# Optimization experiments

Measured on AMD Instinct MI355X. Metric: run time of the kernel, lower is better.

Reference implementation:

```python
import jax, jax.numpy as jnp
import numpy as np

RATE = 2
KSIZE = 3          # patch size for similarity
KERNEL = 2 * RATE  # patch size for alpha scatter (4)
BN_EPS = 1e-5


def _extract_patches(x, k, s):
    """Mirror of GuidedCxtAtten.extract_patches: reflect-pad then unfold.
    x: [B,C,H,W] -> [B,Ho,Wo,C,k,k] with Ho=H//s, Wo=W//s."""
    left = (k - s + 1) // 2
    right = (k - s) // 2
    xp = jnp.pad(x, ((0, 0), (0, 0), (left, right), (left, right)), mode='reflect')
    Hp, Wp = xp.shape[2], xp.shape[3]
    Ho = (Hp - k) // s + 1
    Wo = (Wp - k) // s + 1
    ii = (jnp.arange(Ho) * s)[:, None] + jnp.arange(k)[None, :]   # [Ho,k]
    jj = (jnp.arange(Wo) * s)[:, None] + jnp.arange(k)[None, :]   # [Wo,k]
    p = xp[:, :, ii[:, :, None, None], jj[None, None, :, :]]      # [B,C,Ho,k,Wo,k]
    return p.transpose(0, 2, 4, 1, 3, 5)                          # [B,Ho,Wo,C,k,k]


def setup_inputs() -> dict:
    key = jax.random.key(0)
    ks = jax.random.split(key, 5)
    B, Cg, Ca, H, W = 4, 256, 128, 128, 128
    f = jax.random.normal(ks[0], (B, Cg, H, W), dtype=jnp.float32)
    alpha = jax.random.normal(ks[1], (B, Ca, H, W), dtype=jnp.float32)
    unknown = (jax.random.uniform(ks[2], (B, 1, H, W)) > 0.5).astype(jnp.float32)
    # guidance_conv: 1x1, Cg -> Cg//2, xavier-ish
    gc_w = jax.random.normal(ks[3], (Cg // 2, Cg), dtype=jnp.float32) * np.sqrt(2.0 / (Cg + Cg // 2))
    gc_b = jnp.zeros((Cg // 2,), dtype=jnp.float32)
    # W[0]: 1x1 conv Ca->Ca no bias; W[1]: BN with gamma=0.001, beta=0 per init
    w_w = jax.random.normal(ks[4], (Ca, Ca), dtype=jnp.float32) * np.sqrt(1.0 / Ca)
    bn_gamma = jnp.full((Ca,), 0.001, dtype=jnp.float32)
    bn_beta = jnp.zeros((Ca,), dtype=jnp.float32)
    return {"f": f, "alpha": alpha, "unknown": unknown, "gc_w": gc_w, "gc_b": gc_b,
            "w_w": w_w, "bn_gamma": bn_gamma, "bn_beta": bn_beta}


def _forward(f, alpha, unknown, gc_w, gc_b, w_w, bn_gamma, bn_beta):
    # guidance 1x1 conv
    fg = jnp.einsum('oi,bihw->bohw', gc_w, f) + gc_b[None, :, None, None]
    B, _, H, W = fg.shape
    Ca = alpha.shape[1]
    Hs, Ws = H // RATE, W // RATE
    L = Hs * Ws

    # alpha patches [B,L,Ca,4,4] (kernel=2*rate, stride=rate)
    alpha_w = _extract_patches(alpha, KERNEL, RATE).reshape(B, L, Ca, KERNEL, KERNEL)

    # nearest downsample by rate (torch nearest with scale 1/2 == strided pick)
    f_ds = fg[:, :, ::RATE, ::RATE]                # [B,Cg/2,Hs,Ws]
    unk_ds = unknown[:, :, ::RATE, ::RATE]         # [B,1,Hs,Ws]

    # similarity filter patches [B,L,C,3,3]
    w = _extract_patches(f_ds, KSIZE, 1).reshape(B, L, -1, KSIZE, KSIZE)

    # known/unknown softmax scales [B,2]
    u_mean = unk_ds.mean(axis=(2, 3))              # [B,1]
    k_mean = 1.0 - u_mean
    su = jnp.clip(jnp.sqrt(u_mean / k_mean), 0.1, 10.0)
    sk = jnp.clip(jnp.sqrt(k_mean / u_mean), 0.1, 10.0)
    softmax_scale = jnp.concatenate([su, sk], axis=1)

    # patch-mean of unknown mask -> binary patch mask [B,L]
    m = _extract_patches(unk_ds, KSIZE, 1).reshape(B, L, -1).mean(axis=2)
    mm = (m > 0.0).astype(fg.dtype)

    # l2-normalize filters per patch, then correlate against all positions.
    # Conv of reflect-padded f_ds with stride-1 3x3 patch filters == inner
    # product of normalized patches with the raw patches (same extraction).
    norm = jnp.sqrt(jnp.sum(w * w, axis=(2, 3, 4), keepdims=True))
    w_normed = w / jnp.maximum(norm, 1e-4)
    scores = jnp.einsum('bqcij,bpcij->bqp', w_normed, w)   # [B,L(q=patch),L(p=pos)]

    # known/unknown scaling per source patch q
    gate = jnp.where(mm > 0.0, su, sk)                      # [B,L]
    scores = scores * gate[:, :, None]

    # self-match suppression only for unknown patches (diagonal q == p)
    diag = jnp.arange(L)
    scores = scores.at[:, diag, diag].add(-10000.0 * mm)

    attn = jax.nn.softmax(scores, axis=1)                   # softmax over patches q

    # offsets (argmax patch per position, relative to center)
    idx = jnp.argmax(attn, axis=1)                          # [B,L]
    offsets = jnp.stack([idx // Ws, idx % Ws], axis=1).reshape(B, 2, Hs, Ws)
    offsets = offsets - jnp.array([Hs // 2, Ws // 2]).reshape(1, 2, 1, 1)

    # scatter alpha patches with attention weights: per-sample conv_transpose2d
    attn_map = attn.reshape(B, L, Hs, Ws)

    def ct(yi, wc):  # yi [L,Hs,Ws], wc [L,Ca,4,4]
        rhs = jnp.flip(wc, (2, 3)).transpose(1, 0, 2, 3)    # [Ca,L,4,4]
        pad = KERNEL - 1 - 1                                # torch padding=1
        out = jax.lax.conv_general_dilated(
            yi[None], rhs, window_strides=(1, 1),
            padding=[(pad, pad), (pad, pad)], lhs_dilation=(RATE, RATE),
            dimension_numbers=('NCHW', 'OIHW', 'NCHW'))
        return out[0]

    y = jax.vmap(ct)(attn_map, alpha_w) / 4.0               # [B,Ca,H,W]

    # W: 1x1 conv (no bias) + BatchNorm2d (training-mode batch stats)
    yw = jnp.einsum('oi,bihw->bohw', w_w, y)
    mean = yw.mean(axis=(0, 2, 3))
    var = yw.var(axis=(0, 2, 3))
    yn = (yw - mean[None, :, None, None]) * jax.lax.rsqrt(var + BN_EPS)[None, :, None, None]
    yn = yn * bn_gamma[None, :, None, None] + bn_beta[None, :, None, None]

    return yn + alpha, offsets, softmax_scale


def reference(f, alpha, unknown, gc_w, gc_b, w_w, bn_gamma, bn_beta):
    return _forward(f, alpha, unknown, gc_w, gc_b, w_w, bn_gamma, bn_beta)
```

## Files before the change

kernel.cpp:

```cpp
#include <hip/hip_runtime.h>
#include <math.h>

#define B 4
#define CG 256
#define CM 128
#define CA 128
#define H 128
#define W_ 128
#define HS 64
#define WS 64
#define L 4096
#define D1 1152
#define D2 2048
#define NPIX 65536
#define NT1 36
#define NT2 128

#define STP_F 8388608UL
#define WF_F  4718592UL
#define ZB_F  4194304UL
#define SLOT_F (STP_F + WF_F + ZB_F)

typedef unsigned short u16;
typedef __attribute__((ext_vector_type(8))) short short8v;
typedef __attribute__((ext_vector_type(4))) unsigned short u16x4;
typedef __attribute__((ext_vector_type(4))) float f32x4;

__device__ __forceinline__ float bf2f(u16 x) {
    union { unsigned int u; float f; } v; v.u = ((unsigned int)x) << 16; return v.f;
}
__device__ __forceinline__ u16 f2bf(float x) {
    union { float f; unsigned int u; } v; v.f = x;
    unsigned int r = (v.u + 0x7FFFu + ((v.u >> 16) & 1u)) >> 16;
    return (u16)r;
}
__device__ __forceinline__ void gll16(const void* g, void* l) {
    __builtin_amdgcn_global_load_lds((const __attribute__((address_space(1))) void*)g,
                                     (__attribute__((address_space(3))) void*)l, 16, 0, 0);
}
__device__ __forceinline__ int refl(int i, int n) {
    return i < 0 ? -i : (i >= n ? 2 * n - 2 - i : i);
}
__device__ __forceinline__ int swz(int row, int fq) {
    return row * 32 + ((fq ^ ((row >> 1) & 3)) * 8);
}
__device__ __forceinline__ short8v rdfrag32(const char* lds, int r, int fq) {
    return *(const short8v*)(lds + r * 64 + ((fq * 16) ^ (((r >> 1) & 3) << 4)));
}

__global__ __launch_bounds__(256) void k_conv_ds(const float* __restrict__ f,
                                                 const float* __restrict__ gw,
                                                 const float* __restrict__ gb,
                                                 float* __restrict__ fds,
                                                 float* __restrict__ ssq) {
    __shared__ float sf[CG * 64];
    __shared__ float part[4][64];
    int t = threadIdx.x;
    int hs = blockIdx.x, b = blockIdx.y;
    const float* fb = f + (size_t)b * CG * H * W_ + (2 * hs) * W_;
    for (int idx = t; idx < CG * 64; idx += 256) {
        int ci = idx >> 6, ws = idx & 63;
        sf[idx] = fb[(size_t)ci * H * W_ + 2 * ws];
    }
    __syncthreads();
    int ws = t & 63;
    int wave = __builtin_amdgcn_readfirstlane(t >> 6);
    const float* gwp = gw + (size_t)(wave * 32) * CG;
    float acc[32];
#pragma unroll
    for (int r = 0; r < 32; ++r) acc[r] = gb[wave * 32 + r];
    for (int ci = 0; ci < CG; ++ci) {
        float fv = sf[ci * 64 + ws];
#pragma unroll
        for (int r = 0; r < 32; ++r) acc[r] += gwp[r * CG + ci] * fv;
    }
    float sq = 0.f;
#pragma unroll
    for (int r = 0; r < 32; ++r) {
        int co = wave * 32 + r;
        fds[(((size_t)b * CM + co) * HS + hs) * WS + ws] = acc[r];
        sq += acc[r] * acc[r];
    }
    part[wave][ws] = sq;
    __syncthreads();
    if (t < 64)
        ssq[((size_t)b * HS + hs) * WS + t] =
            part[0][t] + part[1][t] + part[2][t] + part[3][t];
}

__global__ __launch_bounds__(256) void k_scale(const float* __restrict__ unk,
                                               float* __restrict__ suk,
                                               float* __restrict__ out2) {
    int b = blockIdx.x, t = threadIdx.x;
    __shared__ float red[256];
    float s = 0.f;
    for (int i = t; i < L; i += 256) {
        int hs = i >> 6, ws = i & 63;
        s += unk[(size_t)b * H * W_ + (2 * hs) * W_ + 2 * ws];
    }
    red[t] = s;
    __syncthreads();
    for (int o = 128; o > 0; o >>= 1) {
        if (t < o) red[t] += red[t + o];
        __syncthreads();
    }
    if (t == 0) {
        float u = red[0] / (float)L;
        float k = 1.0f - u;
        float su = sqrtf(u / k); su = fminf(fmaxf(su, 0.1f), 10.0f);
        float sk = sqrtf(k / u); sk = fminf(fmaxf(sk, 0.1f), 10.0f);
        suk[b * 2] = su; suk[b * 2 + 1] = sk;
        out2[b * 2] = su; out2[b * 2 + 1] = sk;
    }
}

__global__ __launch_bounds__(64) void k_gate(const float* __restrict__ unk,
                                             const float* __restrict__ ssq,
                                             const float* __restrict__ suk,
                                             float* __restrict__ g,
                                             float* __restrict__ dg) {
    int ws = threadIdx.x, hs = blockIdx.x, b = blockIdx.y;
    float sm = 0.f, sq = 0.f;
    for (int di = -1; di <= 1; ++di) {
        int rh = refl(hs + di, HS);
        for (int dj = -1; dj <= 1; ++dj) {
            int rw = refl(ws + dj, WS);
            sm += unk[(size_t)b * H * W_ + (2 * rh) * W_ + 2 * rw];
            sq += ssq[((size_t)b * HS + rh) * WS + rw];
        }
    }
    float mm   = (sm > 0.0f) ? 1.0f : 0.0f;
    float norm = sqrtf(sq);
    float gate = (mm > 0.0f) ? suk[2 * b] : suk[2 * b + 1];
    int q = hs * WS + ws;
    g[(size_t)b * L + q]  = gate / fmaxf(norm, 1e-4f);
    dg[(size_t)b * L + q] = -10000.0f * mm;
}

__global__ __launch_bounds__(256) void k_buildW(const float* __restrict__ fds,
                                                float* __restrict__ base, int b0) {
    int bz = blockIdx.z;
    int b  = b0 + bz;
    float* S   = base + (size_t)bz * SLOT_F;
    float* Wf  = S + STP_F;
    u16*   Whi = (u16*)(S + STP_F + WF_F);
    int ws = threadIdx.x;
    int c  = blockIdx.y * 4 + threadIdx.y;
    int hs = blockIdx.x;
    int q = hs * WS + ws;
    size_t bo = (size_t)q * D1 + c * 9;
    const float* src = fds + ((size_t)b * CM + c) * HS * WS;
#pragma unroll
    for (int i = 0; i < 3; ++i) {
        int rh = refl(hs + i - 1, HS);
#pragma unroll
        for (int j = 0; j < 3; ++j) {
            int rw = refl(ws + j - 1, WS);
            float v = src[rh * WS + rw];
            Wf[bo + i * 3 + j]  = v;
            Whi[bo + i * 3 + j] = f2bf(v);
        }
    }
}

__global__ __launch_bounds__(256) void k_gemm1(float* __restrict__ base,
                                               const float* __restrict__ g0,
                                               const float* __restrict__ dg0,
                                               int b0) {
    __shared__ u16 sA[3][128 * 32], sB[3][128 * 32];
    int bz = blockIdx.z;
    float* S = base + (size_t)bz * SLOT_F;
    u16* STP = (u16*)S;
    const u16* Whi = (const u16*)(S + STP_F + WF_F);
    const float* g  = g0  + (size_t)(b0 + bz) * L;
    const float* dg = dg0 + (size_t)(b0 + bz) * L;

    int tid = threadIdx.x;
    int wv = tid >> 6, lane = tid & 63;
    int t0 = blockIdx.x, I = 0;
    while (t0 >= 32 - I) { t0 -= 32 - I; ++I; }
    int J = I + t0;
    int pTile = I * 128, qTile = J * 128;
    int wp = (wv >> 1) * 64, wq = (wv & 1) * 64;
    int r0 = wv * 32;
    int lrow = lane >> 2;
    int csw = ((lane & 3) ^ ((lrow >> 1) & 3)) * 8;
    int fr = lane & 15, fq = lane >> 4;

    const u16* gArow = Whi + (size_t)(pTile + r0 + lrow) * D1 + csw;
    const u16* gBrow = Whi + (size_t)(qTile + r0 + lrow) * D1 + csw;

#define G1STAGE(kt, bf) do { \
    gll16(gArow + (kt) * 32, &sA[bf][r0 * 32]); \
    gll16(gArow + (kt) * 32 + (size_t)16 * D1, &sA[bf][(r0 + 16) * 32]); \
    gll16(gBrow + (kt) * 32, &sB[bf][r0 * 32]); \
    gll16(gBrow + (kt) * 32 + (size_t)16 * D1, &sB[bf][(r0 + 16) * 32]); } while (0)

    f32x4 acc[4][4];
#pragma unroll
    for (int mi = 0; mi < 4; ++mi)
#pragma unroll
        for (int ni = 0; ni < 4; ++ni)
#pragma unroll
            for (int r = 0; r < 4; ++r) acc[mi][ni][r] = 0.f;

    G1STAGE(0, 0);
    G1STAGE(1, 1);
    asm volatile("s_waitcnt vmcnt(4)" ::: "memory");
    __builtin_amdgcn_s_barrier();
    __builtin_amdgcn_sched_barrier(0);

    for (int t = 0; t < NT1; ++t) {
        int cur = t % 3;
        short8v ah[4], bh[4];
#pragma unroll
        for (int i = 0; i < 4; ++i) {
            ah[i] = *(const short8v*)&sA[cur][swz(wp + i * 16 + fr, fq)];
            bh[i] = *(const short8v*)&sB[cur][swz(wq + i * 16 + fr, fq)];
        }
        __builtin_amdgcn_s_setprio(1);
#pragma unroll
        for (int mi = 0; mi < 2; ++mi)
#pragma unroll
            for (int ni = 0; ni < 4; ++ni)
                acc[mi][ni] = __builtin_amdgcn_mfma_f32_16x16x32_bf16(ah[mi], bh[ni], acc[mi][ni], 0, 0, 0);
        __builtin_amdgcn_s_setprio(0);
        int kt2 = (t + 2 < NT1) ? (t + 2) : 0;
        G1STAGE(kt2, (t + 2) % 3);
        asm volatile("s_waitcnt vmcnt(4)" ::: "memory");
        __builtin_amdgcn_sched_barrier(0);
        __builtin_amdgcn_s_setprio(1);
#pragma unroll
        for (int mi = 2; mi < 4; ++mi)
#pragma unroll
            for (int ni = 0; ni < 4; ++ni)
                acc[mi][ni] = __builtin_amdgcn_mfma_f32_16x16x32_bf16(ah[mi], bh[ni], acc[mi][ni], 0, 0, 0);
        __builtin_amdgcn_s_setprio(0);
        __builtin_amdgcn_s_barrier();
        __builtin_amdgcn_sched_barrier(0);
    }
#undef G1STAGE

#pragma unroll
    for (int ni = 0; ni < 4; ++ni) {
        int qq = qTile + wq + ni * 16 + fr;
        float gq = g[qq];
        float dq = dg[qq];
#pragma unroll
        for (int mi = 0; mi < 4; ++mi) {
            int pB = pTile + wp + mi * 16 + fq * 4;
#pragma unroll
            for (int r = 0; r < 4; ++r) {
                int p = pB + r;
                float v = acc[mi][ni][r] * gq;
                if (p == qq) v += dq;
                STP[(size_t)p * L + qq] = f2bf(v);
            }
        }
    }
    if (I != J) {
#pragma unroll
        for (int mi = 0; mi < 4; ++mi) {
            int p0 = pTile + wp + mi * 16 + fq * 4;
            float gp0 = g[p0], gp1 = g[p0 + 1], gp2 = g[p0 + 2], gp3 = g[p0 + 3];
#pragma unroll
            for (int ni = 0; ni < 4; ++ni) {
                int qq = qTile + wq + ni * 16 + fr;
                u16x4 mv;
                mv[0] = f2bf(acc[mi][ni][0] * gp0);
                mv[1] = f2bf(acc[mi][ni][1] * gp1);
                mv[2] = f2bf(acc[mi][ni][2] * gp2);
                mv[3] = f2bf(acc[mi][ni][3] * gp3);
                *(u16x4*)(STP + (size_t)qq * L + p0) = mv;
            }
        }
    }
}

__global__ __launch_bounds__(256) void k_softmax(float* __restrict__ base,
                                                 const float* __restrict__ g0,
                                                 const float* __restrict__ dg0,
                                                 float* __restrict__ out1, int b0) {
    __shared__ float buf[L];
    __shared__ float wmax[4], wsum[4], cred[4];
    __shared__ int candList[128];
    __shared__ int candCount;
    int bz = blockIdx.y;
    int b  = b0 + bz;
    float* S = base + (size_t)bz * SLOT_F;
    u16* STP = (u16*)S;
    const float* Wf = S + STP_F;
    const float* g  = g0  + (size_t)b * L;
    const float* dg = dg0 + (size_t)b * L;

    int p = blockIdx.x, t = threadIdx.x;
    int lane = t & 63, wv = t >> 6;
    u16* rowp = STP + (size_t)p * L;

    if (t == 0) candCount = 0;
    float mx = -3.4e38f;
    for (int i = t; i < L / 8; i += 256) {
        short8v v8 = ((const short8v*)rowp)[i];
#pragma unroll
        for (int j = 0; j < 8; ++j) {
            float v = bf2f((u16)v8[j]);
            buf[i * 8 + j] = v;
            mx = fmaxf(mx, v);
        }
    }
#pragma unroll
    for (int o = 32; o > 0; o >>= 1) mx = fmaxf(mx, __shfl_xor(mx, o));
    if (lane == 0) wmax[wv] = mx;
    __syncthreads();
    float M = fmaxf(fmaxf(wmax[0], wmax[1]), fmaxf(wmax[2], wmax[3]));
    float cth = M - (fabsf(M) * 0.0625f + 1e-5f);

    float s = 0.f;
    for (int i = t; i < L; i += 256) {
        float v = buf[i];
        if (v >= cth) {
            int ix = atomicAdd(&candCount, 1);
            if (ix < 128) candList[ix] = i;
        }
        float e = __expf(v - M);
        buf[i] = e;
        s += e;
    }
#pragma unroll
    for (int o = 32; o > 0; o >>= 1) s += __shfl_xor(s, o);
    if (lane == 0) wsum[wv] = s;
    __syncthreads();
    float inv = 1.0f / (wsum[0] + wsum[1] + wsum[2] + wsum[3]);

    for (int i = t; i < L / 8; i += 256) {
        short8v o8;
#pragma unroll
        for (int j = 0; j < 8; ++j) o8[j] = (short)f2bf(buf[i * 8 + j] * inv);
        ((short8v*)rowp)[i] = o8;
    }

    int nc = candCount; if (nc > 128) nc = 128;
    int bestI;
    if (nc == 1) {
        bestI = candList[0];
    } else {
        float bestE = -3.4e38f; bestI = L;
        const float* wp_ = Wf + (size_t)p * D1;
        for (int k = 0; k < nc; ++k) {
            int cand = candList[k];
            const float* wc = Wf + (size_t)cand * D1;
            float part = 0.f;
            for (int j = t; j < D1; j += 256) part += wp_[j] * wc[j];
#pragma unroll
            for (int o = 32; o > 0; o >>= 1) part += __shfl_xor(part, o);
            if (lane == 0) cred[wv] = part;
            __syncthreads();
            float e1 = (cred[0] + cred[1] + cred[2] + cred[3]) * g[cand]
                     + (p == cand ? dg[cand] : 0.f);
            if (e1 > bestE || (e1 == bestE && cand < bestI)) { bestE = e1; bestI = cand; }
            __syncthreads();
        }
    }
    if (t == 0) {
        out1[(size_t)(b * 2 + 0) * L + p] = (float)(bestI / WS - 32);
        out1[(size_t)(b * 2 + 1) * L + p] = (float)(bestI % WS - 32);
    }
}

__global__ __launch_bounds__(256) void k_buildA(const float* __restrict__ alpha,
                                                float* __restrict__ base, int b0) {
    int bz = blockIdx.z;
    int b  = b0 + bz;
    u16* At = (u16*)(base + (size_t)bz * SLOT_F + STP_F);
    int q = blockIdx.x * 256 + threadIdx.x;
    int n = blockIdx.y;
    int hs = q >> 6, ws = q & 63;
    int c = n >> 4, ki = (n >> 2) & 3, kj = n & 3;
    int rh = refl(2 * hs + ki - 1, H);
    int rw = refl(2 * ws + kj - 1, W_);
    At[(size_t)n * L + q] = f2bf(alpha[((size_t)b * CA + c) * H * W_ + rh * W_ + rw]);
}

__global__ __launch_bounds__(512, 2) void k_gemm2(float* __restrict__ base) {
    __shared__ u16 smem[65536];
    char* sm = (char*)smem;
    int bz = blockIdx.z;
    float* S = base + (size_t)bz * SLOT_F;
    const u16* P  = (const u16*)S;
    const u16* At = (const u16*)(S + STP_F);
    u16* Z        = (u16*)(S + STP_F + WF_F);

    int tid = threadIdx.x;
    int wid = tid >> 6, lane = tid & 63;
    int wm = wid >> 2, wn = wid & 3;
    int pTile = blockIdx.x * 256, nTile = blockIdx.y * 256;
    int fr = lane & 15, fq = lane >> 4;

    int off0 = wid * 1024 + lane * 16;
    int row0 = off0 >> 6, cb0 = off0 & 63;
    int off1 = off0 + 8192;
    int row1 = off1 >> 6, cb1 = off1 & 63;
    const u16* pA0 = P  + (size_t)(pTile + row0) * L + ((cb0 ^ (((row0 >> 1) & 3) << 4)) >> 1);
    const u16* pA1 = P  + (size_t)(pTile + row1) * L + ((cb1 ^ (((row1 >> 1) & 3) << 4)) >> 1);
    const u16* pB0 = At + (size_t)(nTile + row0) * L + ((cb0 ^ (((row0 >> 1) & 3) << 4)) >> 1);
    const u16* pB1 = At + (size_t)(nTile + row1) * L + ((cb1 ^ (((row1 >> 1) & 3) << 4)) >> 1);

#define STG2(kt, bi) do { \
    char* d = sm + (bi) * 32768 + wid * 1024; \
    gll16(pA0 + (size_t)(kt) * 32, d); \
    gll16(pA1 + (size_t)(kt) * 32, d + 8192); \
    gll16(pB0 + (size_t)(kt) * 32, d + 16384); \
    gll16(pB1 + (size_t)(kt) * 32, d + 24576); } while (0)

#define PRELOAD2(fa, fb, bi) do { \
    const char* Ab_ = sm + (bi) * 32768; \
    const char* Bb_ = Ab_ + 16384; \
    _Pragma("unroll") for (int n = 0; n < 4; ++n) fb[n] = rdfrag32(Bb_, wn * 64 + n * 16 + fr, fq); \
    _Pragma("unroll") for (int m = 0; m < 8; ++m) fa[m] = rdfrag32(Ab_, wm * 128 + m * 16 + fr, fq); } while (0)

#define PHASE2(t, ca, cb, na, nb_) do { \
    const char* Abn = sm + (((t) + 1) & 3) * 32768; \
    const char* Bbn = Abn + 16384; \
    _Pragma("unroll") for (int n = 0; n < 4; ++n) nb_[n] = rdfrag32(Bbn, wn * 64 + n * 16 + fr, fq); \
    __builtin_amdgcn_s_setprio(1); \
    _Pragma("unroll") for (int m = 0; m < 4; ++m) \
        _Pragma("unroll") for (int n = 0; n < 4; ++n) \
            acc[m][n] = __builtin_amdgcn_mfma_f32_16x16x32_bf16(ca[m], cb[n], acc[m][n], 0, 0, 0); \
    __builtin_amdgcn_s_setprio(0); \
    _Pragma("unroll") for (int m = 0; m < 8; ++m) na[m] = rdfrag32(Abn, wm * 128 + m * 16 + fr, fq); \
    STG2(((t) + 3 < NT2) ? (t) + 3 : 0, ((t) + 3) & 3); \
    asm volatile("s_waitcnt vmcnt(4)" ::: "memory"); \
    __builtin_amdgcn_s_setprio(1); \
    _Pragma("unroll") for (int m = 4; m < 8; ++m) \
        _Pragma("unroll") for (int n = 0; n < 4; ++n) \
            acc[m][n] = __builtin_amdgcn_mfma_f32_16x16x32_bf16(ca[m], cb[n], acc[m][n], 0, 0, 0); \
    __builtin_amdgcn_s_setprio(0); \
    asm volatile("s_waitcnt lgkmcnt(0)" ::: "memory"); \
    __builtin_amdgcn_s_barrier(); \
    __builtin_amdgcn_sched_barrier(0); } while (0)

    f32x4 acc[8][4];
#pragma unroll
    for (int m = 0; m < 8; ++m)
#pragma unroll
        for (int n = 0; n < 4; ++n)
#pragma unroll
            for (int r = 0; r < 4; ++r) acc[m][n][r] = 0.f;

    STG2(0, 0);
    STG2(1, 1);
    STG2(2, 2);
    asm volatile("s_waitcnt vmcnt(4)" ::: "memory");
    __builtin_amdgcn_s_barrier();
    __builtin_amdgcn_sched_barrier(0);

    short8v fa0[8], fb0[4], fa1[8], fb1[4];
    PRELOAD2(fa0, fb0, 0);
    asm volatile("s_waitcnt lgkmcnt(0)" ::: "memory");
    __builtin_amdgcn_sched_barrier(0);

    for (int t = 0; t < NT2; t += 2) {
        PHASE2(t,     fa0, fb0, fa1, fb1);
        PHASE2(t + 1, fa1, fb1, fa0, fb0);
    }
#undef PHASE2
#undef PRELOAD2
#undef STG2

#pragma unroll
    for (int m = 0; m < 8; ++m)
#pragma unroll
        for (int n = 0; n < 4; ++n) {
            int nn = nTile + wn * 64 + n * 16 + fr;
#pragma unroll
            for (int r = 0; r < 4; ++r) {
                int pp = pTile + wm * 128 + m * 16 + fq * 4 + r;
                Z[(size_t)pp * D2 + nn] = f2bf(acc[m][n][r]);
            }
        }
}

__global__ __launch_bounds__(256) void k_gather(float* __restrict__ base,
                                                u16* __restrict__ yt, int b0) {
    int bz = blockIdx.z;
    int b  = b0 + bz;
    const u16* Z = (const u16*)(base + (size_t)bz * SLOT_F + STP_F + WF_F);
    int c  = threadIdx.x & 127;
    int pl = threadIdx.x >> 7;
    int w  = blockIdx.x * 2 + pl;
    int h  = blockIdx.y;
    float s = 0.f;
#pragma unroll
    for (int ki = 0; ki < 4; ++ki) {
        int num = h + 1 - ki;
        if (num < 0 || (num & 1)) continue;
        int hs = num >> 1;
        if (hs >= HS) continue;
#pragma unroll
        for (int kj = 0; kj < 4; ++kj) {
            int numw = w + 1 - kj;
            if (numw < 0 || (numw & 1)) continue;
            int wsd = numw >> 1;
            if (wsd >= WS) continue;
            s += bf2f(Z[(size_t)(hs * WS + wsd) * D2 + c * 16 + ki * 4 + kj]);
        }
    }
    int pix = h * W_ + w;
    int cs = c ^ ((pix & 7) << 3);
    yt[((size_t)b * 16384 + pix) * 128 + cs] = f2bf(0.25f * s);
}

__global__ __launch_bounds__(256) void k_cvtww(const float* __restrict__ ww,
                                               u16* __restrict__ wwbf) {
    int i = blockIdx.x * 256 + threadIdx.x;
    int o = i >> 7, c = i & 127;
    wwbf[o * 128 + (c ^ ((o & 7) << 3))] = f2bf(ww[i]);
}

__global__ __launch_bounds__(256) void k_ywgemm(const u16* __restrict__ wwbf,
                                                const u16* __restrict__ yt,
                                                float* __restrict__ yw) {
    __shared__ u16 sA[128 * 128], sB[128 * 128];
    int tid = threadIdx.x;
    int wv = tid >> 6, lane = tid & 63;
    int nTile = blockIdx.x * 128;
    int wp = (wv >> 1) * 64, wn = (wv & 1) * 64;
    int fr = lane & 15, fq = lane >> 4;

    const u16* gB = yt + (size_t)nTile * 128;
#pragma unroll
    for (int i = 0; i < 8; ++i) {
        int o = (i * 4 + wv) * 512;
        gll16(wwbf + o + lane * 8, &sA[o]);
        gll16(gB + o + lane * 8, &sB[o]);
    }
    __syncthreads();

    f32x4 acc[4][4];
#pragma unroll
    for (int mi = 0; mi < 4; ++mi)
#pragma unroll
        for (int ni = 0; ni < 4; ++ni)
#pragma unroll
            for (int r = 0; r < 4; ++r) acc[mi][ni][r] = 0.f;

#pragma unroll
    for (int ks = 0; ks < 4; ++ks) {
        int k0 = ks * 32 + fq * 8;
        short8v a[4], bb[4];
#pragma unroll
        for (int i = 0; i < 4; ++i) {
            int ra = wp + i * 16 + fr;
            a[i] = *(const short8v*)&sA[ra * 128 + (k0 ^ ((ra & 7) << 3))];
            int rb = wn + i * 16 + fr;
            bb[i] = *(const short8v*)&sB[rb * 128 + (k0 ^ ((rb & 7) << 3))];
        }
#pragma unroll
        for (int mi = 0; mi < 4; ++mi)
#pragma unroll
            for (int ni = 0; ni < 4; ++ni)
                acc[mi][ni] = __builtin_amdgcn_mfma_f32_16x16x32_bf16(a[mi], bb[ni], acc[mi][ni], 0, 0, 0);
    }

#pragma unroll
    for (int mi = 0; mi < 4; ++mi)
#pragma unroll
        for (int ni = 0; ni < 4; ++ni) {
            int gp = nTile + wn + ni * 16 + fr;
#pragma unroll
            for (int r = 0; r < 4; ++r) {
                int o = wp + mi * 16 + fq * 4 + r;
                yw[(size_t)o * NPIX + gp] = acc[mi][ni][r];
            }
        }
}

__global__ __launch_bounds__(256) void k_stats(const float* __restrict__ yw,
                                               float* __restrict__ meanvar) {
    int o = blockIdx.x, t = threadIdx.x;
    __shared__ float rs[256], rq[256];
    float s = 0.f, q = 0.f;
    const float* p = yw + (size_t)o * NPIX;
    for (int i = t; i < NPIX; i += 256) {
        float v = p[i];
        s += v;
        q += v * v;
    }
    rs[t] = s; rq[t] = q;
    __syncthreads();
    for (int off = 128; off > 0; off >>= 1) {
        if (t < off) { rs[t] += rs[t + off]; rq[t] += rq[t + off]; }
        __syncthreads();
    }
    if (t == 0) {
        float n = (float)NPIX;
        float mean = rs[0] / n;
        float var  = rq[0] / n - mean * mean;
        meanvar[o] = mean;
        meanvar[CA + o] = var;
    }
}

__global__ __launch_bounds__(256) void k_final(const float* __restrict__ yw,
                                               const float* __restrict__ meanvar,
                                               const float* __restrict__ gamma,
                                               const float* __restrict__ beta,
                                               const float* __restrict__ alpha,
                                               float* __restrict__ out0) {
    size_t i = ((size_t)blockIdx.x * 256 + threadIdx.x) * 4;
    int c = (int)((i >> 14) & 127);
    int b = (int)(i >> 21);
    int pix = (int)(i & 16383);
    float4 v = *(const float4*)(yw + (size_t)c * NPIX + b * 16384 + pix);
    float4 a = *(const float4*)(alpha + i);
    float mean = meanvar[c];
    float var  = meanvar[CA + c];
    float sc   = rsqrtf(var + 1e-5f) * gamma[c];
    float bt   = beta[c];
    float4 r;
    r.x = (v.x - mean) * sc + bt + a.x;
    r.y = (v.y - mean) * sc + bt + a.y;
    r.z = (v.z - mean) * sc + bt + a.z;
    r.w = (v.w - mean) * sc + bt + a.w;
    *(float4*)(out0 + i) = r;
}

extern "C" void kernel_launch(void* const* d_in, const int* in_sizes, int n_in,
                              void* d_out, int out_size, void* d_ws, size_t ws_size,
                              hipStream_t stream) {
    (void)in_sizes; (void)n_in; (void)out_size;
    const float* f     = (const float*)d_in[0];
    const float* alpha = (const float*)d_in[1];
    const float* unk   = (const float*)d_in[2];
    const float* gw    = (const float*)d_in[3];
    const float* gb    = (const float*)d_in[4];
    const float* ww    = (const float*)d_in[5];
    const float* gamma = (const float*)d_in[6];
    const float* beta  = (const float*)d_in[7];

    float* out0 = (float*)d_out;
    float* out1 = out0 + (size_t)B * CA * H * W_;
    float* out2 = out1 + (size_t)B * 2 * HS * WS;

    float* wsf = (float*)d_ws;
    size_t off = 0;
    float* fds     = wsf + off; off += (size_t)B * CM * HS * WS;
    float* ssq     = wsf + off; off += (size_t)B * HS * WS;
    float* gbuf    = wsf + off; off += (size_t)B * L;
    float* dgbuf   = wsf + off; off += (size_t)B * L;
    float* suk     = wsf + off; off += 64;
    float* ytF     = wsf + off; off += (size_t)NPIX * 128 / 2;
    float* wwbfF   = wsf + off; off += 8192;
    float* meanvar = wsf + off; off += 256;
    float* base    = wsf + off;

    const size_t PRE_F = off;
    int nb = (ws_size >= (PRE_F + 4 * SLOT_F) * sizeof(float)) ? 4 : 2;

    float* yw   = base;
    u16*   yt   = (u16*)ytF;
    u16*   wwbf = (u16*)wwbfF;

    k_cvtww<<<64, 256, 0, stream>>>(ww, wwbf);
    k_conv_ds<<<dim3(64, 4), 256, 0, stream>>>(f, gw, gb, fds, ssq);
    k_scale<<<4, 256, 0, stream>>>(unk, suk, out2);
    k_gate<<<dim3(64, 4), 64, 0, stream>>>(unk, ssq, suk, gbuf, dgbuf);

    for (int b0 = 0; b0 < B; b0 += nb) {
        k_buildW<<<dim3(64, 32, nb), dim3(64, 4), 0, stream>>>(fds, base, b0);
        k_gemm1<<<dim3(528, 1, nb), 256, 0, stream>>>(base, gbuf, dgbuf, b0);
        k_softmax<<<dim3(4096, nb), 256, 0, stream>>>(base, gbuf, dgbuf, out1, b0);
        k_buildA<<<dim3(16, 2048, nb), 256, 0, stream>>>(alpha, base, b0);
        k_gemm2<<<dim3(16, 8, nb), 512, 0, stream>>>(base);
        k_gather<<<dim3(64, 128, nb), 256, 0, stream>>>(base, yt, b0);
    }

    k_ywgemm<<<512, 256, 0, stream>>>(wwbf, yt, yw);
    k_stats<<<128, 256, 0, stream>>>(yw, meanvar);
    k_final<<<8192, 256, 0, stream>>>(yw, meanvar, gamma, beta, alpha, out0);
}
```

Measured before the change: 843.8 us.

## Drop fp32 patch buffer, recompute from fds, and prefetch LDS fragments in gemm1

The fp32 unfolded patch matrix Wf is no longer materialised. The softmax tie-break dot products now gather directly from the downsampled feature map using reflect indexing, which shrinks the per-sample workspace slot and removes a large fp32 write in buildW. The gemm1 main loop is restructured to keep three stages in flight and double-buffer the register fragments, loading the next tile's LDS fragments while MFMAs on the current tile run. It also adds an occupancy hint of 3 blocks per SM.

New measurement: 829.9 us. About the same (-1.7%).

```diff
diff --git a/kernel.cpp b/kernel.cpp
--- a/kernel.cpp
+++ b/kernel.cpp
@@ -17,9 +17,8 @@
 #define NT2 128
 
 #define STP_F 8388608UL
-#define WF_F  4718592UL
-#define ZB_F  4194304UL
-#define SLOT_F (STP_F + WF_F + ZB_F)
+#define RA_F  4194304UL
+#define SLOT_F (STP_F + RA_F + RA_F)
 
 typedef unsigned short u16;
 typedef __attribute__((ext_vector_type(8))) short short8v;
@@ -141,9 +140,7 @@
                                                 float* __restrict__ base, int b0) {
     int bz = blockIdx.z;
     int b  = b0 + bz;
-    float* S   = base + (size_t)bz * SLOT_F;
-    float* Wf  = S + STP_F;
-    u16*   Whi = (u16*)(S + STP_F + WF_F);
+    u16* Whi = (u16*)(base + (size_t)bz * SLOT_F + STP_F);
     int ws = threadIdx.x;
     int c  = blockIdx.y * 4 + threadIdx.y;
     int hs = blockIdx.x;
@@ -156,22 +153,20 @@
 #pragma unroll
         for (int j = 0; j < 3; ++j) {
             int rw = refl(ws + j - 1, WS);
-            float v = src[rh * WS + rw];
-            Wf[bo + i * 3 + j]  = v;
-            Whi[bo + i * 3 + j] = f2bf(v);
-        }
-    }
-}
-
-__global__ __launch_bounds__(256) void k_gemm1(float* __restrict__ base,
-                                               const float* __restrict__ g0,
-                                               const float* __restrict__ dg0,
-                                               int b0) {
+            Whi[bo + i * 3 + j] = f2bf(src[rh * WS + rw]);
+        }
+    }
+}
+
+__global__ __launch_bounds__(256, 3) void k_gemm1(float* __restrict__ base,
+                                                  const float* __restrict__ g0,
+                                                  const float* __restrict__ dg0,
+                                                  int b0) {
     __shared__ u16 sA[3][128 * 32], sB[3][128 * 32];
     int bz = blockIdx.z;
     float* S = base + (size_t)bz * SLOT_F;
     u16* STP = (u16*)S;
-    const u16* Whi = (const u16*)(S + STP_F + WF_F);
+    const u16* Whi = (const u16*)(S + STP_F);
     const float* g  = g0  + (size_t)(b0 + bz) * L;
     const float* dg = dg0 + (size_t)(b0 + bz) * L;
 
@@ -190,12 +185,34 @@
     const u16* gArow = Whi + (size_t)(pTile + r0 + lrow) * D1 + csw;
     const u16* gBrow = Whi + (size_t)(qTile + r0 + lrow) * D1 + csw;
 
-#define G1STAGE(kt, bf) do { \
+#define G1STG(kt, bf) do { \
     gll16(gArow + (kt) * 32, &sA[bf][r0 * 32]); \
     gll16(gArow + (kt) * 32 + (size_t)16 * D1, &sA[bf][(r0 + 16) * 32]); \
     gll16(gBrow + (kt) * 32, &sB[bf][r0 * 32]); \
     gll16(gBrow + (kt) * 32 + (size_t)16 * D1, &sB[bf][(r0 + 16) * 32]); } while (0)
 
+#define G1PHASE(t, ca, cb, na, nb_) do { \
+    int nxb = ((t) + 1) % 3; \
+    _Pragma("unroll") for (int i = 0; i < 4; ++i) \
+        nb_[i] = *(const short8v*)&sB[nxb][swz(wq + i * 16 + fr, fq)]; \
+    __builtin_amdgcn_s_setprio(1); \
+    _Pragma("unroll") for (int mi = 0; mi < 2; ++mi) \
+        _Pragma("unroll") for (int ni = 0; ni < 4; ++ni) \
+            acc[mi][ni] = __builtin_amdgcn_mfma_f32_16x16x32_bf16(ca[mi], cb[ni], acc[mi][ni], 0, 0, 0); \
+    __builtin_amdgcn_s_setprio(0); \
+    _Pragma("unroll") for (int i = 0; i < 4; ++i) \
+        na[i] = *(const short8v*)&sA[nxb][swz(wp + i * 16 + fr, fq)]; \
+    G1STG(((t) + 3 < NT1) ? (t) + 3 : 0, (t) % 3); \
+    asm volatile("s_waitcnt vmcnt(4)" ::: "memory"); \
+    __builtin_amdgcn_s_setprio(1); \
+    _Pragma("unroll") for (int mi = 2; mi < 4; ++mi) \
+        _Pragma("unroll") for (int ni = 0; ni < 4; ++ni) \
+            acc[mi][ni] = __builtin_amdgcn_mfma_f32_16x16x32_bf16(ca[mi], cb[ni], acc[mi][ni], 0, 0, 0); \
+    __builtin_amdgcn_s_setprio(0); \
+    asm volatile("s_waitcnt lgkmcnt(0)" ::: "memory"); \
+    __builtin_amdgcn_s_barrier(); \
+    __builtin_amdgcn_sched_barrier(0); } while (0)
+
     f32x4 acc[4][4];
 #pragma unroll
     for (int mi = 0; mi < 4; ++mi)
@@ -204,42 +221,29 @@
 #pragma unroll
             for (int r = 0; r < 4; ++r) acc[mi][ni][r] = 0.f;
 
-    G1STAGE(0, 0);
-    G1STAGE(1, 1);
+    G1STG(0, 0);
+    G1STG(1, 1);
+    G1STG(2, 2);
     asm volatile("s_waitcnt vmcnt(4)" ::: "memory");
     __builtin_amdgcn_s_barrier();
     __builtin_amdgcn_sched_barrier(0);
 
-    for (int t = 0; t < NT1; ++t) {
-        int cur = t % 3;
-        short8v ah[4], bh[4];
-#pragma unroll
-        for (int i = 0; i < 4; ++i) {
-            ah[i] = *(const short8v*)&sA[cur][swz(wp + i * 16 + fr, fq)];
-            bh[i] = *(const short8v*)&sB[cur][swz(wq + i * 16 + fr, fq)];
-        }
-        __builtin_amdgcn_s_setprio(1);
-#pragma unroll
-        for (int mi = 0; mi < 2; ++mi)
-#pragma unroll
-            for (int ni = 0; ni < 4; ++ni)
-                acc[mi][ni] = __builtin_amdgcn_mfma_f32_16x16x32_bf16(ah[mi], bh[ni], acc[mi][ni], 0, 0, 0);
-        __builtin_amdgcn_s_setprio(0);
-        int kt2 = (t + 2 < NT1) ? (t + 2) : 0;
-        G1STAGE(kt2, (t + 2) % 3);
-        asm volatile("s_waitcnt vmcnt(4)" ::: "memory");
-        __builtin_amdgcn_sched_barrier(0);
-        __builtin_amdgcn_s_setprio(1);
-#pragma unroll
-        for (int mi = 2; mi < 4; ++mi)
-#pragma unroll
-            for (int ni = 0; ni < 4; ++ni)
-                acc[mi][ni] = __builtin_amdgcn_mfma_f32_16x16x32_bf16(ah[mi], bh[ni], acc[mi][ni], 0, 0, 0);
-        __builtin_amdgcn_s_setprio(0);
-        __builtin_amdgcn_s_barrier();
-        __builtin_amdgcn_sched_barrier(0);
-    }
-#undef G1STAGE
+    short8v fa0[4], fb0[4], fa1[4], fb1[4];
+#pragma unroll
+    for (int i = 0; i < 4; ++i) {
+        fa0[i] = *(const short8v*)&sA[0][swz(wp + i * 16 + fr, fq)];
+        fb0[i] = *(const short8v*)&sB[0][swz(wq + i * 16 + fr, fq)];
+    }
+    asm volatile("s_waitcnt lgkmcnt(0)" ::: "memory");
+    __builtin_amdgcn_s_barrier();
+    __builtin_amdgcn_sched_barrier(0);
+
+    for (int t = 0; t < NT1; t += 2) {
+        G1PHASE(t,     fa0, fb0, fa1, fb1);
+        G1PHASE(t + 1, fa1, fb1, fa0, fb0);
+    }
+#undef G1PHASE
+#undef G1STG
 
 #pragma unroll
     for (int ni = 0; ni < 4; ++ni) {
@@ -278,6 +282,7 @@
 }
 
 __global__ __launch_bounds__(256) void k_softmax(float* __restrict__ base,
+                                                 const float* __restrict__ fds,
                                                  const float* __restrict__ g0,
                                                  const float* __restrict__ dg0,
                                                  float* __restrict__ out1, int b0) {
@@ -289,7 +294,7 @@
     int b  = b0 + bz;
     float* S = base + (size_t)bz * SLOT_F;
     u16* STP = (u16*)S;
-    const float* Wf = S + STP_F;
+    const float* fdsb = fds + (size_t)b * CM * HS * WS;
     const float* g  = g0  + (size_t)b * L;
     const float* dg = dg0 + (size_t)b * L;
 
@@ -345,12 +350,24 @@
         bestI = candList[0];
     } else {
         float bestE = -3.4e38f; bestI = L;
-        const float* wp_ = Wf + (size_t)p * D1;
+        int hp = p >> 6, wpp = p & 63;
         for (int k = 0; k < nc; ++k) {
             int cand = candList[k];
-            const float* wc = Wf + (size_t)cand * D1;
+            int hc = cand >> 6, wcc = cand & 63;
             float part = 0.f;
-            for (int j = t; j < D1; j += 256) part += wp_[j] * wc[j];
+#pragma unroll
+            for (int e = 0; e < 5; ++e) {
+                int kk = t + e * 256;
+                if (kk < D1) {
+                    int c  = kk / 9, ij = kk - c * 9;
+                    int di = ij / 3, dj = ij - di * 3;
+                    float pv = fdsb[(size_t)c * (HS * WS)
+                                    + refl(hp + di - 1, HS) * WS + refl(wpp + dj - 1, WS)];
+                    float cv = fdsb[(size_t)c * (HS * WS)
+                                    + refl(hc + di - 1, HS) * WS + refl(wcc + dj - 1, WS)];
+                    part += pv * cv;
+                }
+            }
 #pragma unroll
             for (int o = 32; o > 0; o >>= 1) part += __shfl_xor(part, o);
             if (lane == 0) cred[wv] = part;
@@ -388,7 +405,7 @@
     float* S = base + (size_t)bz * SLOT_F;
     const u16* P  = (const u16*)S;
     const u16* At = (const u16*)(S + STP_F);
-    u16* Z        = (u16*)(S + STP_F + WF_F);
+    u16* Z        = (u16*)(S + STP_F + RA_F);
 
     int tid = threadIdx.x;
     int wid = tid >> 6, lane = tid & 63;
@@ -484,7 +501,7 @@
                                                 u16* __restrict__ yt, int b0) {
     int bz = blockIdx.z;
     int b  = b0 + bz;
-    const u16* Z = (const u16*)(base + (size_t)bz * SLOT_F + STP_F + WF_F);
+    const u16* Z = (const u16*)(base + (size_t)bz * SLOT_F + STP_F + RA_F);
     int c  = threadIdx.x & 127;
     int pl = threadIdx.x >> 7;
     int w  = blockIdx.x * 2 + pl;
@@ -669,7 +686,7 @@
     for (int b0 = 0; b0 < B; b0 += nb) {
         k_buildW<<<dim3(64, 32, nb), dim3(64, 4), 0, stream>>>(fds, base, b0);
         k_gemm1<<<dim3(528, 1, nb), 256, 0, stream>>>(base, gbuf, dgbuf, b0);
-        k_softmax<<<dim3(4096, nb), 256, 0, stream>>>(base, gbuf, dgbuf, out1, b0);
+        k_softmax<<<dim3(4096, nb), 256, 0, stream>>>(base, fds, gbuf, dgbuf, out1, b0);
         k_buildA<<<dim3(16, 2048, nb), 256, 0, stream>>>(alpha, base, b0);
         k_gemm2<<<dim3(16, 8, nb), 512, 0, stream>>>(base);
         k_gather<<<dim3(64, 128, nb), 256, 0, stream>>>(base, yt, b0);
```
